# Optimization experiments

Measured on AMD Instinct MI355X. Metric: run time of the kernel, lower is better.

## Reference

```python
import jax, jax.numpy as jnp
import numpy as np

B, T, E, H = 1, 4096, 768, 12
DH = E // H


def setup_inputs() -> dict:
    key = jax.random.key(0)
    ks = jax.random.split(key, 10)
    s = 0.02
    inp = {
        "queries": jax.random.normal(ks[0], (B, T, E), jnp.float32),
        "values": jax.random.normal(ks[1], (B, T, E), jnp.float32),
        # causal mask (1 = keep, 0 = masked), matches masked_fill(mask == 0, -1e9)
        "mask": jnp.tril(jnp.ones((T, T), jnp.int32))[None, None, :, :],
        "Wq": jax.random.normal(ks[2], (E, E), jnp.float32) * s,
        "bq": jnp.zeros((E,), jnp.float32),
        "Wk": jax.random.normal(ks[3], (E, E), jnp.float32) * s,
        "bk": jnp.zeros((E,), jnp.float32),
        "Wv": jax.random.normal(ks[4], (E, E), jnp.float32) * s,
        "bv": jnp.zeros((E,), jnp.float32),
        "Wo": jax.random.normal(ks[5], (E, E), jnp.float32) * s,
        "bo": jnp.zeros((E,), jnp.float32),
    }
    return inp


def _split_heads(x):
    # [B,T,E] -> [B,H,T,DH]
    return x.reshape(B, T, H, DH).transpose(0, 2, 1, 3)


def reference(queries, values, mask, Wq, bq, Wk, bk, Wv, bv, Wo, bo):
    # torch nn.Linear: y = x @ W.T + b
    q = _split_heads(queries @ Wq.T + bq)
    k = _split_heads(values @ Wk.T + bk)
    v = _split_heads(values @ Wv.T + bv)
    scale = 1.0 / np.sqrt(DH).astype(np.float32)
    logits = jnp.einsum("bhqd,bhkd->bhqk", q, k) * scale  # [B,H,T,T]
    logits = jnp.where(mask == 0, jnp.float32(-1e9), logits)
    probs = jax.nn.softmax(logits, axis=-1)
    ctx = jnp.einsum("bhqk,bhkd->bhqd", probs, v)  # [B,H,T,DH]
    ctx = ctx.transpose(0, 2, 1, 3).reshape(B, T, E)
    return ctx @ Wo.T + bo
```

## Files before the change

kernel.cpp:

```cpp
#include <hip/hip_runtime.h>
#include <hip/hip_bf16.h>


typedef __hip_bfloat16 bf16;
typedef __attribute__((ext_vector_type(8))) short short8;
typedef __attribute__((ext_vector_type(4))) short short4v;
typedef __attribute__((ext_vector_type(4))) float f32x4;

#define TSEQ 4096
#define NHEAD 12
#define DHEAD 64
#define EMB 768

#if defined(__HIP_DEVICE_COMPILE__)
#define MFMA16(a, b, c) __builtin_amdgcn_mfma_f32_16x16x16bf16_1k(a, b, c, 0, 0, 0)
#else
#define MFMA16(a, b, c) (c)
#endif

typedef const __attribute__((address_space(1))) unsigned int* gptr_t;
typedef __attribute__((address_space(3))) unsigned int* lptr_t;

__device__ __forceinline__ void load_lds16(const void* g, void* l) {
    __builtin_amdgcn_global_load_lds((gptr_t)g, (lptr_t)l, 16, 0, 0);
}

__device__ __forceinline__ float b2f(short s) {
    unsigned u = ((unsigned)(unsigned short)s) << 16;
    float f;
    __builtin_memcpy(&f, &u, 4);
    return f;
}

__device__ __forceinline__ short f2bs(float f) {
    bf16 h = __float2bfloat16(f);
    short s;
    __builtin_memcpy(&s, &h, 2);
    return s;
}

struct CvtJob { const float* src; bf16* dst; int n; };
struct CvtArgs { CvtJob j[4]; };

__global__ __launch_bounds__(256) void cvt_kernel(CvtArgs a) {
    const CvtJob jb = a.j[blockIdx.y];
    const int i = (blockIdx.x * 256 + threadIdx.x) * 8;
    if (i >= jb.n) return;
    const float4 x0 = *(const float4*)(jb.src + i);
    const float4 x1 = *(const float4*)(jb.src + i + 4);
    bf16 tmp[8];
    tmp[0] = __float2bfloat16(x0.x); tmp[1] = __float2bfloat16(x0.y);
    tmp[2] = __float2bfloat16(x0.z); tmp[3] = __float2bfloat16(x0.w);
    tmp[4] = __float2bfloat16(x1.x); tmp[5] = __float2bfloat16(x1.y);
    tmp[6] = __float2bfloat16(x1.z); tmp[7] = __float2bfloat16(x1.w);
    *(short8*)(jb.dst + i) = *(const short8*)tmp;
}

template<int NF, bool AF32>
__device__ __forceinline__ void gemm_t(
    const bf16* __restrict__ A, const float* __restrict__ Af,
    const bf16* __restrict__ W, const float* __restrict__ bias,
    bf16* __restrict__ outb, float* __restrict__ outf,
    const int mode, const float scale, const int m0, const int n0,
    bf16* sA, bf16* sB)
{
    const int tid  = threadIdx.x;
    const int lane = tid & 63;
    const int wave = tid >> 6;
    const int wr = wave >> 1, wc = wave & 1;
    const int lg = lane >> 4, lr = lane & 15;

    f32x4 acc[4][NF];
#pragma unroll
    for (int m = 0; m < 4; ++m)
#pragma unroll
        for (int n = 0; n < NF; ++n)
            acc[m][n] = (f32x4){0.f, 0.f, 0.f, 0.f};

    for (int k0 = 0; k0 < EMB; k0 += 64) {
        if (k0) __syncthreads();
        if constexpr (AF32) {
#pragma unroll
            for (int is = 0; is < 4; ++is) {
                const int chunk = is * 256 + tid;
                const int row = chunk >> 3;
                const int c = chunk & 7;
                const float* src = Af + (size_t)(m0 + row) * EMB + k0 + c * 8;
                const float4 x0 = *(const float4*)src;
                const float4 x1 = *(const float4*)(src + 4);
                bf16 t8[8];
                t8[0] = __float2bfloat16(x0.x); t8[1] = __float2bfloat16(x0.y);
                t8[2] = __float2bfloat16(x0.z); t8[3] = __float2bfloat16(x0.w);
                t8[4] = __float2bfloat16(x1.x); t8[5] = __float2bfloat16(x1.y);
                t8[6] = __float2bfloat16(x1.z); t8[7] = __float2bfloat16(x1.w);
                *(short8*)(sA + row * 64 + ((c ^ (row & 7)) * 8)) = *(const short8*)t8;
            }
        } else {
#pragma unroll
            for (int is = 0; is < 4; ++is) {
                const int chunk = is * 256 + tid;
                const int row = chunk >> 3;
                const int csw = (chunk & 7) ^ (row & 7);
                load_lds16(A + (size_t)(m0 + row) * EMB + k0 + csw * 8,
                           sA + is * 2048 + wave * 512);
            }
        }
#pragma unroll
        for (int is = 0; is < NF; ++is) {
            const int chunk = is * 256 + tid;
            const int row = chunk >> 3;
            const int csw = (chunk & 7) ^ (row & 7);
            load_lds16(W + (size_t)(n0 + row) * EMB + k0 + csw * 8,
                       sB + is * 2048 + wave * 512);
        }
        __syncthreads();

        short8 af[4][2], bfv[NF][2];
#pragma unroll
        for (int m = 0; m < 4; ++m)
#pragma unroll
            for (int kk = 0; kk < 2; ++kk) {
                const int row = wr * 64 + m * 16 + lr;
                const int cc = (kk * 4 + lg) ^ (row & 7);
                af[m][kk] = *(const short8*)(sA + row * 64 + cc * 8);
            }
#pragma unroll
        for (int n = 0; n < NF; ++n)
#pragma unroll
            for (int kk = 0; kk < 2; ++kk) {
                const int row = wc * (NF * 16) + n * 16 + lr;
                const int cc = (kk * 4 + lg) ^ (row & 7);
                bfv[n][kk] = *(const short8*)(sB + row * 64 + cc * 8);
            }
#pragma unroll
        for (int kk = 0; kk < 2; ++kk)
#pragma unroll
            for (int m = 0; m < 4; ++m)
#pragma unroll
                for (int n = 0; n < NF; ++n)
                    acc[m][n] = __builtin_amdgcn_mfma_f32_16x16x32_bf16(
                        af[m][kk], bfv[n][kk], acc[m][n], 0, 0, 0);
    }

#pragma unroll
    for (int n = 0; n < NF; ++n) {
        const int o = n0 + wc * (NF * 16) + n * 16 + lr;
        const float bv = bias[o];
#pragma unroll
        for (int m = 0; m < 4; ++m) {
            const int tbase = m0 + wr * 64 + m * 16 + lg * 4;
#pragma unroll
            for (int r = 0; r < 4; ++r) {
                const float v = (acc[m][n][r] + bv) * scale;
                const int t = tbase + r;
                if (mode == 0)
                    outb[(size_t)(o >> 6) * TSEQ * DHEAD + (size_t)t * DHEAD + (o & 63)] =
                        __float2bfloat16(v);
                else if (mode == 1)
                    outb[(size_t)(o >> 6) * DHEAD * TSEQ + (size_t)(o & 63) * TSEQ + t] =
                        __float2bfloat16(v);
                else
                    outf[(size_t)t * EMB + o] = v;
            }
        }
    }
}

struct QkvArgs {
    const float *xq, *xv;
    const bf16 *Wq, *Wk, *Wv;
    const float *bq, *bk, *bv;
    bf16 *qo, *ko, *vto;
};

__global__ __launch_bounds__(256) void qkv_gemm(QkvArgs a) {
    __shared__ __attribute__((aligned(16))) bf16 sA[128 * 64];
    __shared__ __attribute__((aligned(16))) bf16 sB[128 * 64];
    const int z = blockIdx.z;
    const float* Af = (z == 0) ? a.xq : a.xv;
    const bf16* W = (z == 0) ? a.Wq : (z == 1 ? a.Wk : a.Wv);
    const float* b = (z == 0) ? a.bq : (z == 1 ? a.bk : a.bv);
    bf16* o = (z == 0) ? a.qo : (z == 1 ? a.ko : a.vto);
    const int mode = (z == 2) ? 1 : 0;
    const float scale = (z == 0) ? 0.18033688011112042f : 1.0f;
    gemm_t<4, true>(nullptr, Af, W, b, o, nullptr, mode, scale,
                    blockIdx.y * 128, blockIdx.x * 128, sA, sB);
}

__global__ __launch_bounds__(256) void out_gemm(
    const bf16* __restrict__ ctx, const bf16* __restrict__ Wo,
    const float* __restrict__ bo, float* __restrict__ out)
{
    __shared__ __attribute__((aligned(16))) bf16 sA[128 * 64];
    __shared__ __attribute__((aligned(16))) bf16 sB[64 * 64];
    gemm_t<2, false>(ctx, nullptr, Wo, bo, nullptr, out, 2, 1.0f,
                     blockIdx.y * 128, blockIdx.x * 64, sA, sB);
}

struct AttnState {
    f32x4 O[4];
    float m, l;
};

__device__ __forceinline__ void stage_tile(
    const bf16* __restrict__ Kh, const bf16* __restrict__ Vh,
    bf16* sK, bf16* sV, const int kv0, const int tid)
{
    const int wave = tid >> 6;
#pragma unroll
    for (int is = 0; is < 2; ++is) {
        const int chunk = is * 256 + tid;
        const int row = chunk >> 3;
        const int csw = (chunk & 7) ^ (row & 7);
        load_lds16(Kh + (size_t)(kv0 + row) * DHEAD + csw * 8,
                   sK + is * 2048 + wave * 512);
        load_lds16(Vh + (size_t)row * TSEQ + kv0 + csw * 8,
                   sV + is * 2048 + wave * 512);
    }
}

template<int BUF>
__device__ __forceinline__ void attn_tile(
    const bf16* kp0, const bf16* kp1,
    const bf16* vp0, const bf16* vp1, const bf16* vp2, const bf16* vp3,
    const short8 (&qf)[2], AttnState& st,
    const int kv0, const int qw, const int lane)
{
    const int lg = lane >> 4, lr = lane & 15;
    if (kv0 > qw + 15) return;

    f32x4 s[4];
    short8 kf[4][2];
#pragma unroll
    for (int n = 0; n < 4; ++n) {
        kf[n][0] = *(const short8*)(kp0 + BUF * 4096 + n * 1024);
        kf[n][1] = *(const short8*)(kp1 + BUF * 4096 + n * 1024);
    }
#pragma unroll
    for (int n = 0; n < 4; ++n) s[n] = (f32x4){0.f, 0.f, 0.f, 0.f};
#pragma unroll
    for (int kk = 0; kk < 2; ++kk)
#pragma unroll
        for (int n = 0; n < 4; ++n)
            s[n] = __builtin_amdgcn_mfma_f32_16x16x32_bf16(
                kf[n][kk], qf[kk], s[n], 0, 0, 0);

    if (kv0 + 63 > qw) {
        const int qi = qw + lr;
#pragma unroll
        for (int n = 0; n < 4; ++n) {
            const int kb = kv0 + n * 16 + lg * 4;
#pragma unroll
            for (int r = 0; r < 4; ++r)
                if (kb + r > qi) s[n][r] = -3.0e38f;
        }
    }

    const float a0 = fmaxf(fmaxf(s[0][0], s[0][1]), fmaxf(s[0][2], s[0][3]));
    const float a1 = fmaxf(fmaxf(s[1][0], s[1][1]), fmaxf(s[1][2], s[1][3]));
    const float a2 = fmaxf(fmaxf(s[2][0], s[2][1]), fmaxf(s[2][2], s[2][3]));
    const float a3 = fmaxf(fmaxf(s[3][0], s[3][1]), fmaxf(s[3][2], s[3][3]));
    float mx = fmaxf(fmaxf(a0, a1), fmaxf(a2, a3));
    mx = fmaxf(mx, __shfl_xor(mx, 16));
    mx = fmaxf(mx, __shfl_xor(mx, 32));

    const float mn = fmaxf(st.m, mx);
    const float al = __builtin_amdgcn_exp2f(st.m - mn);
    st.m = mn;

    float rsn[4];
    short4v pq[4];
#pragma unroll
    for (int n = 0; n < 4; ++n) {
        const float p0 = __builtin_amdgcn_exp2f(s[n][0] - mn);
        const float p1 = __builtin_amdgcn_exp2f(s[n][1] - mn);
        const float p2 = __builtin_amdgcn_exp2f(s[n][2] - mn);
        const float p3 = __builtin_amdgcn_exp2f(s[n][3] - mn);
        rsn[n] = (p0 + p1) + (p2 + p3);
        pq[n][0] = f2bs(p0); pq[n][1] = f2bs(p1);
        pq[n][2] = f2bs(p2); pq[n][3] = f2bs(p3);
    }
    float rs = (rsn[0] + rsn[1]) + (rsn[2] + rsn[3]);
    rs += __shfl_xor(rs, 16);
    rs += __shfl_xor(rs, 32);
    st.l = st.l * al + rs;

#pragma unroll
    for (int nd = 0; nd < 4; ++nd)
#pragma unroll
        for (int r = 0; r < 4; ++r)
            st.O[nd][r] *= al;

#pragma unroll
    for (int nd = 0; nd < 4; ++nd) {
        f32x4 o = st.O[nd];
        o = MFMA16(*(const short4v*)(vp0 + BUF * 4096 + nd * 1024), pq[0], o);
        o = MFMA16(*(const short4v*)(vp1 + BUF * 4096 + nd * 1024), pq[1], o);
        o = MFMA16(*(const short4v*)(vp2 + BUF * 4096 + nd * 1024), pq[2], o);
        o = MFMA16(*(const short4v*)(vp3 + BUF * 4096 + nd * 1024), pq[3], o);
        st.O[nd] = o;
    }
}

__global__ __launch_bounds__(256, 4) void attn_kernel(
    const bf16* __restrict__ Q, const bf16* __restrict__ K,
    const bf16* __restrict__ VT, bf16* __restrict__ Opart,
    float* __restrict__ ml, const int nch_max, const int U)
{
    __shared__ __attribute__((aligned(16))) bf16 sK[2][64 * 64];
    __shared__ __attribute__((aligned(16))) bf16 sV[2][64 * 64];

    const int tid  = threadIdx.x;
    const int lane = tid & 63;
    const int wave = tid >> 6;
    const int lg = lane >> 4, lr = lane & 15;

    const int bid = blockIdx.x;
    const int h = bid % 12;
    int rem = (U - 1) - (bid / 12);
    int g = 0;
    while (g < 7) {
        const int cap = (g + 1 < nch_max) ? g + 1 : nch_max;
        const int gu = 8 * cap;
        if (rem < gu) break;
        rem -= gu;
        ++g;
    }
    const int d = (g + 1 < nch_max) ? g + 1 : nch_max;
    const int bx = 8 * g + rem / d;
    const int c = rem % d;

    const int q0 = bx * 64;
    const int qw = q0 + wave * 16;
    const int S = bx + 1;
    const int t0 = (c * S) / d;
    const int t1 = ((c + 1) * S) / d;

    const bf16* Qh = Q  + (size_t)h * TSEQ * DHEAD;
    const bf16* Kh = K  + (size_t)h * TSEQ * DHEAD;
    const bf16* Vh = VT + (size_t)h * DHEAD * TSEQ;

    short8 qf[2];
#pragma unroll
    for (int kk = 0; kk < 2; ++kk)
        qf[kk] = *(const short8*)(Qh + (size_t)(qw + lr) * DHEAD + kk * 32 + lg * 8);

    const int kb0 = lr * 64 + ((lg ^ (lr & 7)) * 8);
    const bf16* kp0 = &sK[0][0] + kb0;
    const bf16* kp1 = &sK[0][0] + (kb0 ^ 32);
    const int vx = ((lg >> 1) ^ (lr & 7)) * 8;
    const int vb = lr * 64 + (lg & 1) * 4;
    const bf16* vp0 = &sV[0][0] + vb + (0 ^ vx);
    const bf16* vp1 = &sV[0][0] + vb + (16 ^ vx);
    const bf16* vp2 = &sV[0][0] + vb + (32 ^ vx);
    const bf16* vp3 = &sV[0][0] + vb + (48 ^ vx);

    AttnState st;
#pragma unroll
    for (int nd = 0; nd < 4; ++nd) st.O[nd] = (f32x4){0.f, 0.f, 0.f, 0.f};
    st.m = -3.0e38f; st.l = 0.f;

    stage_tile(Kh, Vh, &sK[0][0], &sV[0][0], t0 * 64, tid);
    __syncthreads();

    int it = t0;
    while (it < t1) {
        if (it + 1 < t1) stage_tile(Kh, Vh, &sK[1][0], &sV[1][0], (it + 1) * 64, tid);
        attn_tile<0>(kp0, kp1, vp0, vp1, vp2, vp3, qf, st, it * 64, qw, lane);
        __syncthreads();
        ++it;
        if (it >= t1) break;
        if (it + 1 < t1) stage_tile(Kh, Vh, &sK[0][0], &sV[0][0], (it + 1) * 64, tid);
        attn_tile<1>(kp0, kp1, vp0, vp1, vp2, vp3, qf, st, it * 64, qw, lane);
        __syncthreads();
        ++it;
    }

    const int u = (h * 64 + bx) * nch_max + c;
    bf16* op = Opart + (size_t)u * 4096;
    float* mlp = ml + (size_t)u * 128;
    const int q = wave * 16 + lr;
#pragma unroll
    for (int nd = 0; nd < 4; ++nd) {
        short4v ov;
        ov[0] = f2bs(st.O[nd][0]); ov[1] = f2bs(st.O[nd][1]);
        ov[2] = f2bs(st.O[nd][2]); ov[3] = f2bs(st.O[nd][3]);
        *(short4v*)(op + q * 64 + nd * 16 + lg * 4) = ov;
    }
    if (lg == 0) {
        mlp[q] = st.m;
        mlp[64 + q] = st.l;
    }
}

__global__ __launch_bounds__(256) void combine_kernel(
    const bf16* __restrict__ Opart, const float* __restrict__ ml,
    bf16* __restrict__ ctx, const int nch_max)
{
    const int h  = blockIdx.y;
    const int bx = blockIdx.x;
    const int tid = threadIdx.x;
    const int row = tid >> 2;
    const int dp  = (tid & 3) * 16;
    const int ub = (h * 64 + bx) * nch_max;
    const int g = bx >> 3;
    const int nchb = (nch_max > 1) ? ((g + 1 < nch_max) ? g + 1 : nch_max) : 1;

    float M = -3.0e38f;
    for (int c = 0; c < nchb; ++c)
        M = fmaxf(M, ml[(size_t)(ub + c) * 128 + row]);

    float L = 0.f;
    float acc[16];
#pragma unroll
    for (int i = 0; i < 16; ++i) acc[i] = 0.f;
    for (int c = 0; c < nchb; ++c) {
        const float mc = ml[(size_t)(ub + c) * 128 + row];
        const float lc = ml[(size_t)(ub + c) * 128 + 64 + row];
        const float w = __builtin_amdgcn_exp2f(mc - M);
        L += lc * w;
        const bf16* op = Opart + ((size_t)(ub + c) * 64 + row) * 64 + dp;
        const short8 v0 = *(const short8*)op;
        const short8 v1 = *(const short8*)(op + 8);
#pragma unroll
        for (int i = 0; i < 8; ++i) acc[i] += w * b2f(v0[i]);
#pragma unroll
        for (int i = 0; i < 8; ++i) acc[8 + i] += w * b2f(v1[i]);
    }
    const float invL = 1.0f / L;

    bf16 outv[16];
#pragma unroll
    for (int i = 0; i < 16; ++i) outv[i] = __float2bfloat16(acc[i] * invL);
    const int t = bx * 64 + row;
    bf16* dst = ctx + (size_t)t * EMB + h * DHEAD + dp;
    *(short8*)dst = *(const short8*)outv;
    *(short8*)(dst + 8) = *(const short8*)(outv + 8);
}

extern "C" void kernel_launch(void* const* d_in, const int* in_sizes, int n_in,
                              void* d_out, int out_size, void* d_ws, size_t ws_size,
                              hipStream_t stream) {
    const float* queries = (const float*)d_in[0];
    const float* values  = (const float*)d_in[1];
    const float* Wq = (const float*)d_in[3];
    const float* bq = (const float*)d_in[4];
    const float* Wk = (const float*)d_in[5];
    const float* bk = (const float*)d_in[6];
    const float* Wv = (const float*)d_in[7];
    const float* bv = (const float*)d_in[8];
    const float* Wo = (const float*)d_in[9];
    const float* bo = (const float*)d_in[10];
    float* out = (float*)d_out;

    const size_t NTE = (size_t)TSEQ * EMB;
    const size_t WSZ = (size_t)EMB * EMB;
    bf16* ws  = (bf16*)d_ws;
    bf16* qb  = ws;
    bf16* vb  = qb + NTE;
    bf16* wqb = vb + NTE;
    bf16* wkb = wqb + WSZ;
    bf16* wvb = wkb + WSZ;
    bf16* wob = wvb + WSZ;
    bf16* qh  = wob + WSZ;
    bf16* kh  = qh + NTE;
    bf16* vth = kh + NTE;
    bf16* ctx = qb;

    const size_t fixed_elems = 5 * NTE + 4 * WSZ;
    int nch = 8;
    for (;;) {
        const size_t units = (size_t)NHEAD * (TSEQ / 64) * nch;
        const size_t need = fixed_elems * 2 + units * 4096 * 2 + units * 128 * 4;
        if (ws_size >= need || nch == 1) break;
        nch = (nch == 8) ? 4 : 1;
    }
    const size_t units = (size_t)NHEAD * (TSEQ / 64) * nch;
    bf16* opart = ws + fixed_elems;
    float* ml = (float*)(opart + units * 4096);

    int U = 0;
    for (int g = 0; g < 8; ++g) U += 8 * ((g + 1 < nch) ? g + 1 : nch);

    CvtArgs ca;
    ca.j[0] = {Wq, wqb, (int)WSZ};
    ca.j[1] = {Wk, wkb, (int)WSZ};
    ca.j[2] = {Wv, wvb, (int)WSZ};
    ca.j[3] = {Wo, wob, (int)WSZ};
    cvt_kernel<<<dim3((WSZ + 2047) / 2048, 4), 256, 0, stream>>>(ca);

    QkvArgs a{queries, values, wqb, wkb, wvb, bq, bk, bv, qh, kh, vth};
    qkv_gemm<<<dim3(EMB / 128, TSEQ / 128, 3), 256, 0, stream>>>(a);
    attn_kernel<<<dim3(12 * U), 256, 0, stream>>>(qh, kh, vth, opart, ml, nch, U);
    combine_kernel<<<dim3(TSEQ / 64, NHEAD), 256, 0, stream>>>(opart, ml, ctx, nch);
    out_gemm<<<dim3(EMB / 64, TSEQ / 128), 256, 0, stream>>>(ctx, wob, bo, out);
}
```

Before: 131.7 us.

## Remap GEMM blocks for XCD locality and skip lazy softmax rescaling

Both projection GEMMs switch to a 1D grid whose block index is remapped so that blocks landing on the same XCD (round-robin by block index modulo 8) share row tiles of the activation matrix, aiming to improve L2 reuse on the multi-die GPU. Separately, the attention inner loop skips the running-max update and the rescaling of O and l when every lane's new tile max lies within 8 (log2 units) of the stored max. This lazy rescaling removes exp and multiply work on most tiles, at the cost of a wave-wide vote and larger unnormalized exponents, up to 2^8, before the final normalization.

```diff
diff --git a/kernel.cpp b/kernel.cpp
--- a/kernel.cpp
+++ b/kernel.cpp
@@ -176,15 +176,21 @@
 __global__ __launch_bounds__(256) void qkv_gemm(QkvArgs a) {
     __shared__ __attribute__((aligned(16))) bf16 sA[128 * 64];
     __shared__ __attribute__((aligned(16))) bf16 sB[128 * 64];
-    const int z = blockIdx.z;
+    const int z = blockIdx.y;
+    const int b = blockIdx.x;
+    const int xcd = b & 7;
+    const int rest = b >> 3;
+    const int cc = rest % 6;
+    const int rg = rest / 6;
+    const int rr = xcd + 8 * rg;
     const float* Af = (z == 0) ? a.xq : a.xv;
     const bf16* W = (z == 0) ? a.Wq : (z == 1 ? a.Wk : a.Wv);
-    const float* b = (z == 0) ? a.bq : (z == 1 ? a.bk : a.bv);
+    const float* bias = (z == 0) ? a.bq : (z == 1 ? a.bk : a.bv);
     bf16* o = (z == 0) ? a.qo : (z == 1 ? a.ko : a.vto);
     const int mode = (z == 2) ? 1 : 0;
     const float scale = (z == 0) ? 0.18033688011112042f : 1.0f;
-    gemm_t<4, true>(nullptr, Af, W, b, o, nullptr, mode, scale,
-                    blockIdx.y * 128, blockIdx.x * 128, sA, sB);
+    gemm_t<4, true>(nullptr, Af, W, bias, o, nullptr, mode, scale,
+                    rr * 128, cc * 128, sA, sB);
 }
 
 __global__ __launch_bounds__(256) void out_gemm(
@@ -193,8 +199,14 @@
 {
     __shared__ __attribute__((aligned(16))) bf16 sA[128 * 64];
     __shared__ __attribute__((aligned(16))) bf16 sB[64 * 64];
+    const int b = blockIdx.x;
+    const int xcd = b & 7;
+    const int rest = b >> 3;
+    const int cc = rest % 12;
+    const int rg = rest / 12;
+    const int rr = xcd + 8 * rg;
     gemm_t<2, false>(ctx, nullptr, Wo, bo, nullptr, out, 2, 1.0f,
-                     blockIdx.y * 128, blockIdx.x * 64, sA, sB);
+                     rr * 128, cc * 64, sA, sB);
 }
 
 struct AttnState {
@@ -264,18 +276,29 @@
     mx = fmaxf(mx, __shfl_xor(mx, 16));
     mx = fmaxf(mx, __shfl_xor(mx, 32));
 
-    const float mn = fmaxf(st.m, mx);
-    const float al = __builtin_amdgcn_exp2f(st.m - mn);
-    st.m = mn;
+    float mref;
+    if (__all(mx <= st.m + 8.0f)) {
+        mref = st.m;
+    } else {
+        mref = fmaxf(st.m, mx);
+        const float al = __builtin_amdgcn_exp2f(st.m - mref);
+        st.m = mref;
+        st.l *= al;
+#pragma unroll
+        for (int nd = 0; nd < 4; ++nd)
+#pragma unroll
+            for (int r = 0; r < 4; ++r)
+                st.O[nd][r] *= al;
+    }
 
     float rsn[4];
     short4v pq[4];
 #pragma unroll
     for (int n = 0; n < 4; ++n) {
-        const float p0 = __builtin_amdgcn_exp2f(s[n][0] - mn);
-        const float p1 = __builtin_amdgcn_exp2f(s[n][1] - mn);
-        const float p2 = __builtin_amdgcn_exp2f(s[n][2] - mn);
-        const float p3 = __builtin_amdgcn_exp2f(s[n][3] - mn);
+        const float p0 = __builtin_amdgcn_exp2f(s[n][0] - mref);
+        const float p1 = __builtin_amdgcn_exp2f(s[n][1] - mref);
+        const float p2 = __builtin_amdgcn_exp2f(s[n][2] - mref);
+        const float p3 = __builtin_amdgcn_exp2f(s[n][3] - mref);
         rsn[n] = (p0 + p1) + (p2 + p3);
         pq[n][0] = f2bs(p0); pq[n][1] = f2bs(p1);
         pq[n][2] = f2bs(p2); pq[n][3] = f2bs(p3);
@@ -283,13 +306,7 @@
     float rs = (rsn[0] + rsn[1]) + (rsn[2] + rsn[3]);
     rs += __shfl_xor(rs, 16);
     rs += __shfl_xor(rs, 32);
-    st.l = st.l * al + rs;
-
-#pragma unroll
-    for (int nd = 0; nd < 4; ++nd)
-#pragma unroll
-        for (int r = 0; r < 4; ++r)
-            st.O[nd][r] *= al;
+    st.l += rs;
 
 #pragma unroll
     for (int nd = 0; nd < 4; ++nd) {
@@ -490,8 +507,8 @@
     cvt_kernel<<<dim3((WSZ + 2047) / 2048, 4), 256, 0, stream>>>(ca);
 
     QkvArgs a{queries, values, wqb, wkb, wvb, bq, bk, bv, qh, kh, vth};
-    qkv_gemm<<<dim3(EMB / 128, TSEQ / 128, 3), 256, 0, stream>>>(a);
+    qkv_gemm<<<dim3(192, 3), 256, 0, stream>>>(a);
     attn_kernel<<<dim3(12 * U), 256, 0, stream>>>(qh, kh, vth, opart, ml, nch, U);
     combine_kernel<<<dim3(TSEQ / 64, NHEAD), 256, 0, stream>>>(opart, ml, ctx, nch);
-    out_gemm<<<dim3(EMB / 64, TSEQ / 128), 256, 0, stream>>>(ctx, wob, bo, out);
-}
+    out_gemm<<<dim3(384), 256, 0, stream>>>(ctx, wob, bo, out);
+}
```

After: 119.2 us. -9.4%, faster.
